# Kernel tuning notes

Measured on AMD Instinct MI355X. Metric: run time of the kernel, lower is better.

The kernel has to match this reference:

```python
import jax, jax.numpy as jnp
import numpy as np

N_NODES = 100000
N_EDGES = 1600000
IN_F = 128
OUT_F = 64
BN_EPS = 1e-5


def setup_inputs() -> dict:
    key = jax.random.key(0)
    ks = jax.random.split(key, 6)
    feature = jax.random.normal(ks[0], (N_NODES, IN_F), dtype=jnp.float32)
    src = jax.random.randint(ks[1], (N_EDGES,), 0, N_NODES, dtype=jnp.int32)
    dst = jax.random.randint(ks[2], (N_EDGES,), 0, N_NODES, dtype=jnp.int32)
    W = jax.random.normal(ks[3], (IN_F, OUT_F), dtype=jnp.float32) * 0.05
    b = jnp.zeros((OUT_F,), dtype=jnp.float32)
    res_W = jax.random.normal(ks[4], (IN_F, OUT_F), dtype=jnp.float32) * 0.05
    res_b = jnp.zeros((OUT_F,), dtype=jnp.float32)
    gamma = jnp.ones((OUT_F,), dtype=jnp.float32)
    beta = jnp.zeros((OUT_F,), dtype=jnp.float32)
    return {"feature": feature, "src": src, "dst": dst, "W": W, "b": b,
            "res_W": res_W, "res_b": res_b, "gamma": gamma, "beta": beta,
            "idx": 0}


def _gcn_layer(feature, src, dst, W, b, res_W, res_b, gamma, beta):
    n = feature.shape[0]
    ones = jnp.ones_like(src, dtype=feature.dtype)
    # DGL norm='both': src-side uses out-degree, dst-side uses in-degree,
    # degrees clamped to min 1 (allow_zero_in_degree=True).
    out_deg = jax.ops.segment_sum(ones, src, num_segments=n)
    in_deg = jax.ops.segment_sum(ones, dst, num_segments=n)
    norm_src = jax.lax.rsqrt(jnp.maximum(out_deg, 1.0))  # [N]
    norm_dst = jax.lax.rsqrt(jnp.maximum(in_deg, 1.0))   # [N]

    # in_feats (128) > out_feats (64): DGL multiplies by W before aggregation.
    h = (feature * norm_src[:, None]) @ W                 # [N, OUT_F]
    agg = jax.ops.segment_sum(h[src], dst, num_segments=n)  # [N, OUT_F]
    conv = jax.nn.relu(agg * norm_dst[:, None] + b)

    # residual connection: activation(Linear(feature))
    res = jax.nn.relu(feature @ res_W + res_b)
    y = conv + res

    # BatchNorm1d (training mode, biased variance)
    mean = jnp.mean(y, axis=0)
    var = jnp.mean(jnp.square(y - mean), axis=0)
    y = (y - mean) * jax.lax.rsqrt(var + BN_EPS) * gamma + beta
    return y


def reference(feature, src, dst, W, b, res_W, res_b, gamma, beta, idx):
    # idx == 0 -> dropout branch is skipped (eval-deterministic reference)
    return _gcn_layer(feature, src, dst, W, b, res_W, res_b, gamma, beta)
```

## Files before the change

### kernel.cpp

```cpp
#include <hip/hip_runtime.h>
#include <hip/hip_fp16.h>

#define NCOL 64
#define KDIM 128
#define NB 512
#define CH 2048

typedef short bf16x8 __attribute__((ext_vector_type(8)));
typedef float f32x4 __attribute__((ext_vector_type(4)));
typedef float f32x2 __attribute__((ext_vector_type(2)));

__device__ __forceinline__ unsigned short f2bf(float f) {
    unsigned int u = __float_as_uint(f);
    return (unsigned short)((u + 0x7fffu + ((u >> 16) & 1u)) >> 16);
}

__global__ __launch_bounds__(256) void coarse_hist(const int* __restrict__ src,
                                                   const int* __restrict__ dst,
                                                   int* __restrict__ outcnt,
                                                   int* __restrict__ bcnt, int E) {
    __shared__ int lh[NB];
    int tid = threadIdx.x;
    for (int i = tid; i < NB; i += 256) lh[i] = 0;
    __syncthreads();
    int i = blockIdx.x * blockDim.x + tid;
    int stride = gridDim.x * blockDim.x;
    for (int e = i; e < E; e += stride) {
        atomicAdd(&outcnt[src[e]], 1);
        atomicAdd(&lh[dst[e] >> 8], 1);
    }
    __syncthreads();
    for (int k = tid; k < NB; k += 256) {
        int c = lh[k];
        if (c) atomicAdd(&bcnt[k], c);
    }
}

__global__ __launch_bounds__(256) void bucket_scan(const int* __restrict__ bcnt,
                                                   int* __restrict__ bbase, int* __restrict__ bcur,
                                                   int* __restrict__ row_start, int N, int E) {
    __shared__ int wsum[8];
    int tid = threadIdx.x, lane = tid & 63, wv = tid >> 6;
    int a = bcnt[tid], b = bcnt[tid + 256];
    int ia = a, ib = b;
#pragma unroll
    for (int off = 1; off < 64; off <<= 1) {
        int t = __shfl_up(ia, off); if (lane >= off) ia += t;
        int u = __shfl_up(ib, off); if (lane >= off) ib += u;
    }
    if (lane == 63) { wsum[wv] = ia; wsum[4 + wv] = ib; }
    __syncthreads();
    if (tid == 0) { int run = 0; for (int i = 0; i < 8; ++i) { int t = wsum[i]; wsum[i] = run; run += t; } }
    __syncthreads();
    int ea = wsum[wv] + ia - a;
    int eb = wsum[4 + wv] + ib - b;
    bbase[tid] = ea; bcur[tid] = ea;
    bbase[tid + 256] = eb; bcur[tid + 256] = eb;
    if (tid == 0) row_start[N] = E;
}

__global__ __launch_bounds__(256) void partition_kernel(
    const int* __restrict__ src, const int* __restrict__ dst,
    int* __restrict__ bcur, uint2* __restrict__ pairs, int E) {
    __shared__ int hist[NB];
    __shared__ int lbase[NB];
    __shared__ int gbase[NB];
    __shared__ int lcur[NB];
    __shared__ uint2 sp[CH];
    __shared__ int wsum[8];

    int tid = threadIdx.x, lane = tid & 63, wv = tid >> 6;
    int c0 = blockIdx.x * CH;
    int cnt = min(CH, E - c0);

    for (int i = tid; i < NB; i += 256) hist[i] = 0;
    __syncthreads();
    for (int i = tid; i < cnt; i += 256)
        atomicAdd(&hist[dst[c0 + i] >> 8], 1);
    __syncthreads();

    {
        int a = hist[tid], b = hist[tid + 256];
        int ia = a, ib = b;
#pragma unroll
        for (int off = 1; off < 64; off <<= 1) {
            int t = __shfl_up(ia, off); if (lane >= off) ia += t;
            int u = __shfl_up(ib, off); if (lane >= off) ib += u;
        }
        if (lane == 63) { wsum[wv] = ia; wsum[4 + wv] = ib; }
        __syncthreads();
        if (tid == 0) { int run = 0; for (int i = 0; i < 8; ++i) { int t = wsum[i]; wsum[i] = run; run += t; } }
        __syncthreads();
        lbase[tid] = wsum[wv] + ia - a;
        lbase[tid + 256] = wsum[4 + wv] + ib - b;
    }
    __syncthreads();

    for (int k = tid; k < NB; k += 256) {
        int c = hist[k];
        gbase[k] = c ? atomicAdd(&bcur[k], c) : 0;
        lcur[k] = lbase[k];
    }
    __syncthreads();

    for (int i = tid; i < cnt; i += 256) {
        int s = src[c0 + i], d = dst[c0 + i];
        int p = atomicAdd(&lcur[d >> 8], 1);
        sp[p] = make_uint2((unsigned)s, (unsigned)d);
    }
    __syncthreads();

    for (int i = tid; i < cnt; i += 256) {
        uint2 p = sp[i];
        int k = (int)(p.y >> 8);
        pairs[gbase[k] + (i - lbase[k])] = p;
    }
}

__global__ __launch_bounds__(256) void fine_kernel(
    const uint2* __restrict__ pairs, const int* __restrict__ bbase,
    int* __restrict__ row_start, int* __restrict__ ssrc, int E, int nbuck, int N) {
    __shared__ int hist[256];
    __shared__ int cur[256];
    __shared__ int wsum[4];
    int k = blockIdx.x;
    int tid = threadIdx.x, lane = tid & 63, wv = tid >> 6;
    int b0 = bbase[k];
    int b1 = (k + 1 < nbuck) ? bbase[k + 1] : E;

    hist[tid] = 0;
    __syncthreads();
    for (int i = b0 + tid; i < b1; i += 256)
        atomicAdd(&hist[pairs[i].y & 255], 1);
    __syncthreads();

    int x = hist[tid], inc = x;
#pragma unroll
    for (int off = 1; off < 64; off <<= 1) {
        int t = __shfl_up(inc, off); if (lane >= off) inc += t;
    }
    if (lane == 63) wsum[wv] = inc;
    __syncthreads();
    if (tid == 0) { int run = 0; for (int i = 0; i < 4; ++i) { int t = wsum[i]; wsum[i] = run; run += t; } }
    __syncthreads();
    int excl = wsum[wv] + inc - x;

    int d = (k << 8) + tid;
    if (d < N) row_start[d] = b0 + excl;
    cur[tid] = b0 + excl;
    __syncthreads();

    for (int i = b0 + tid; i < b1; i += 256) {
        uint2 p = pairs[i];
        int pos = atomicAdd(&cur[p.y & 255], 1);
        ssrc[pos] = (int)p.x;
    }
}

__global__ __launch_bounds__(256) void matmul_mfma(
    const float* __restrict__ feat, const float* __restrict__ W,
    const float* __restrict__ RW, const float* __restrict__ res_b,
    const int* __restrict__ outcnt,
    unsigned int* __restrict__ hb8, float* __restrict__ y, int N) {
    __shared__ bf16x8 Bf[2048];
    int tid = threadIdx.x;
    for (int idx = tid; idx < 2048; idx += 256) {
        int mat = idx >> 10;
        int kc = (idx >> 8) & 3;
        int ct = (idx >> 6) & 3;
        int l = idx & 63;
        const float* Wp = mat ? RW : W;
        int kbase = kc * 32 + (l >> 4) * 8;
        int col = ct * 16 + (l & 15);
        bf16x8 t;
#pragma unroll
        for (int j = 0; j < 8; ++j)
            t[j] = (short)f2bf(Wp[(size_t)(kbase + j) * NCOL + col]);
        Bf[idx] = t;
    }
    __syncthreads();

    int lane = tid & 63;
    int wid = tid >> 6;
    int wave = blockIdx.x * 4 + wid;
    int nwaves = gridDim.x * 4;
    int ntiles = (N + 15) >> 4;
    int c16 = lane & 15, kg = lane >> 4;

    float rbv[4];
#pragma unroll
    for (int ct = 0; ct < 4; ++ct) rbv[ct] = res_b[ct * 16 + c16];

    for (int tile = wave; tile < ntiles; tile += nwaves) {
        int tb = tile << 4;
        f32x4 acch[4], accr[4];
#pragma unroll
        for (int ct = 0; ct < 4; ++ct) {
            acch[ct] = (f32x4){0.f, 0.f, 0.f, 0.f};
            accr[ct] = (f32x4){0.f, 0.f, 0.f, 0.f};
        }

        int arow = tb + c16; if (arow >= N) arow = N - 1;
        const float* fp = feat + (size_t)arow * KDIM + kg * 8;
#pragma unroll
        for (int kc = 0; kc < 4; ++kc) {
            float4 a0 = *(const float4*)(fp + kc * 32);
            float4 a1 = *(const float4*)(fp + kc * 32 + 4);
            bf16x8 af;
            af[0] = (short)f2bf(a0.x); af[1] = (short)f2bf(a0.y);
            af[2] = (short)f2bf(a0.z); af[3] = (short)f2bf(a0.w);
            af[4] = (short)f2bf(a1.x); af[5] = (short)f2bf(a1.y);
            af[6] = (short)f2bf(a1.z); af[7] = (short)f2bf(a1.w);
#pragma unroll
            for (int ct = 0; ct < 4; ++ct) {
                acch[ct] = __builtin_amdgcn_mfma_f32_16x16x32_bf16(
                    af, Bf[(kc * 4 + ct) * 64 + lane], acch[ct], 0, 0, 0);
                accr[ct] = __builtin_amdgcn_mfma_f32_16x16x32_bf16(
                    af, Bf[1024 + (kc * 4 + ct) * 64 + lane], accr[ct], 0, 0, 0);
            }
        }

        float nrm[4];
#pragma unroll
        for (int r = 0; r < 4; ++r) {
            int rw = tb + kg * 4 + r; if (rw >= N) rw = N - 1;
            nrm[r] = rsqrtf(fmaxf((float)outcnt[rw], 1.0f));
        }
#pragma unroll
        for (int r = 0; r < 4; ++r) {
            int row = tb + kg * 4 + r;
            if (row < N) {
                unsigned int p = 0;
                p = (unsigned int)__builtin_amdgcn_cvt_pk_fp8_f32(
                        acch[0][r] * nrm[r], acch[1][r] * nrm[r], (int)p, false);
                p = (unsigned int)__builtin_amdgcn_cvt_pk_fp8_f32(
                        acch[2][r] * nrm[r], acch[3][r] * nrm[r], (int)p, true);
#pragma unroll
                for (int ct = 0; ct < 4; ++ct)
                    y[(size_t)row * NCOL + ct * 16 + c16] = fmaxf(accr[ct][r] + rbv[ct], 0.0f);
                hb8[(size_t)row * 16 + c16] = p;
            }
        }
    }
}

#define GATHER_ROW_STEP(eBase, eEnd, A0, A1, A2, A3)                                   \
    {                                                                                   \
        int e0 = (eBase) + e4, e1 = e0 + 4;                                             \
        int i0 = (e0 < (eEnd)) ? ssrc[e0] : -1;                                         \
        int i1 = (e1 < (eEnd)) ? ssrc[e1] : -1;                                         \
        unsigned int v0 = (i0 >= 0) ? hb8[(size_t)i0 * 16 + dw] : 0u;                   \
        unsigned int v1 = (i1 >= 0) ? hb8[(size_t)i1 * 16 + dw] : 0u;                   \
        f32x2 l0 = __builtin_amdgcn_cvt_pk_f32_fp8((int)v0, false);                     \
        f32x2 h0 = __builtin_amdgcn_cvt_pk_f32_fp8((int)v0, true);                      \
        f32x2 l1 = __builtin_amdgcn_cvt_pk_f32_fp8((int)v1, false);                     \
        f32x2 h1 = __builtin_amdgcn_cvt_pk_f32_fp8((int)v1, true);                      \
        A0 += l0[0] + l1[0]; A1 += l0[1] + l1[1];                                       \
        A2 += h0[0] + h1[0]; A3 += h0[1] + h1[1];                                       \
    }

__global__ __launch_bounds__(256) void gather_kernel(
    const int* __restrict__ row_start, const int* __restrict__ ssrc,
    const unsigned int* __restrict__ hb8, const float* __restrict__ b,
    float* __restrict__ y, float* __restrict__ stats, int N) {
    int tid = threadIdx.x, lane = tid & 63, wid = tid >> 6;
    int e4 = lane >> 4, dw = lane & 15;
    int rowSel = e4 >> 1;
    int colLo = ((e4 & 1) << 5) + dw;
    int wave = blockIdx.x * 4 + wid;
    int nwaves = gridDim.x * 4;

    float bcLo = b[colLo], bcHi = b[colLo + 16];
    float bnLo = 0.f, bnHi = 0.f, bnsqLo = 0.f, bnsqHi = 0.f;

    for (int d0 = wave * 2; d0 < N; d0 += 2 * nwaves) {
        int d1 = d0 + 1;
        int a0 = row_start[d0], a1 = row_start[d0 + 1];
        int b0e = 0, b1e = 0;
        if (d1 < N) { b0e = a1; b1e = row_start[d1 + 1]; }

        float A0 = 0.f, A1 = 0.f, A2 = 0.f, A3 = 0.f;
        float B0 = 0.f, B1 = 0.f, B2 = 0.f, B3 = 0.f;
        int nit = max((a1 - a0 + 7) >> 3, (b1e - b0e + 7) >> 3);
        for (int it = 0; it < nit; ++it) {
            GATHER_ROW_STEP(a0 + it * 8, a1, A0, A1, A2, A3)
            GATHER_ROW_STEP(b0e + it * 8, b1e, B0, B1, B2, B3)
        }

#pragma unroll
        for (int off = 16; off <= 32; off <<= 1) {
            A0 += __shfl_xor(A0, off); A1 += __shfl_xor(A1, off);
            A2 += __shfl_xor(A2, off); A3 += __shfl_xor(A3, off);
            B0 += __shfl_xor(B0, off); B1 += __shfl_xor(B1, off);
            B2 += __shfl_xor(B2, off); B3 += __shfl_xor(B3, off);
        }

        int dd = d0 + rowSel;
        if (dd < N) {
            int deg = rowSel ? (b1e - b0e) : (a1 - a0);
            float nd = rsqrtf(fmaxf((float)deg, 1.0f));
            float vLo = rowSel ? ((e4 & 1) ? B2 : B0) : ((e4 & 1) ? A2 : A0);
            float vHi = rowSel ? ((e4 & 1) ? B3 : B1) : ((e4 & 1) ? A3 : A1);
            float* yp = &y[(size_t)dd * NCOL + colLo];
            float v0 = fmaxf(vLo * nd + bcLo, 0.f) + yp[0];
            float v1 = fmaxf(vHi * nd + bcHi, 0.f) + yp[16];
            yp[0] = v0;
            yp[16] = v1;
            bnLo += v0; bnsqLo += v0 * v0;
            bnHi += v1; bnsqHi += v1 * v1;
        }
    }

    bnLo += __shfl_xor(bnLo, 32); bnsqLo += __shfl_xor(bnsqLo, 32);
    bnHi += __shfl_xor(bnHi, 32); bnsqHi += __shfl_xor(bnsqHi, 32);

    __shared__ float bnred[4][128];
    if (lane < 32) {
        bnred[wid][colLo] = bnLo;
        bnred[wid][colLo + 16] = bnHi;
        bnred[wid][64 + colLo] = bnsqLo;
        bnred[wid][64 + colLo + 16] = bnsqHi;
    }
    __syncthreads();
    if (tid < 128) {
        float v = bnred[0][tid] + bnred[1][tid] + bnred[2][tid] + bnred[3][tid];
        unsafeAtomicAdd(&stats[tid], v);
    }
}

__global__ void bnparam_kernel(const float* __restrict__ gamma, const float* __restrict__ beta,
                               float* __restrict__ stats, float invN) {
    int c = threadIdx.x;
    float mean = stats[c] * invN;
    float var = stats[64 + c] * invN - mean * mean;
    float s = gamma[c] * rsqrtf(var + 1e-5f);
    stats[128 + c] = s;
    stats[192 + c] = beta[c] - mean * s;
}

__global__ __launch_bounds__(256) void apply_kernel(float* __restrict__ y,
                                                    const float* __restrict__ stats, int total4) {
    int i = blockIdx.x * blockDim.x + threadIdx.x;
    int stride = gridDim.x * blockDim.x;
    float4* y4 = (float4*)y;
    for (; i < total4; i += stride) {
        float4 v = y4[i];
        int cbase = (i & 15) << 2;
        float4 s = *(const float4*)&stats[128 + cbase];
        float4 t = *(const float4*)&stats[192 + cbase];
        v.x = v.x * s.x + t.x;
        v.y = v.y * s.y + t.y;
        v.z = v.z * s.z + t.z;
        v.w = v.w * s.w + t.w;
        y4[i] = v;
    }
}

extern "C" void kernel_launch(void* const* d_in, const int* in_sizes, int n_in,
                              void* d_out, int out_size, void* d_ws, size_t ws_size,
                              hipStream_t stream) {
    const float* feat  = (const float*)d_in[0];
    const int*   src   = (const int*)d_in[1];
    const int*   dst   = (const int*)d_in[2];
    const float* W     = (const float*)d_in[3];
    const float* b     = (const float*)d_in[4];
    const float* RW    = (const float*)d_in[5];
    const float* rb    = (const float*)d_in[6];
    const float* gamma = (const float*)d_in[7];
    const float* beta  = (const float*)d_in[8];

    int N = in_sizes[0] / KDIM;
    int E = in_sizes[1];
    float* out = (float*)d_out;
    int nbuck = (N + 255) >> 8;

    char* wsb = (char*)d_ws;
    unsigned int* hb8 = (unsigned int*)wsb;                wsb += (size_t)N * 16 * 4;
    uint2* pairs    = (uint2*)wsb;                         wsb += (size_t)E * 8;
    int*   ssrc     = (int*)wsb;                           wsb += (size_t)E * 4;
    int*   row_start= (int*)wsb;                           wsb += (size_t)(N + 1) * 4;
    int*   outcnt   = (int*)wsb;                           wsb += (size_t)N * 4;
    float* stats    = (float*)wsb;                         wsb += 256 * 4;
    int*   bcnt     = (int*)wsb;                           wsb += NB * 4;
    int*   bbase    = (int*)wsb;                           wsb += NB * 4;
    int*   bcur     = (int*)wsb;

    hipMemsetAsync(outcnt, 0, ((size_t)N + 256 + NB) * 4, stream);

    coarse_hist<<<1024, 256, 0, stream>>>(src, dst, outcnt, bcnt, E);
    bucket_scan<<<1, 256, 0, stream>>>(bcnt, bbase, bcur, row_start, N, E);
    matmul_mfma<<<512, 256, 0, stream>>>(feat, W, RW, rb, outcnt, hb8, out, N);
    partition_kernel<<<(E + CH - 1) / CH, 256, 0, stream>>>(src, dst, bcur, pairs, E);
    fine_kernel<<<nbuck, 256, 0, stream>>>(pairs, bbase, row_start, ssrc, E, nbuck, N);
    gather_kernel<<<2048, 256, 0, stream>>>(row_start, ssrc, hb8, b, out, stats, N);
    bnparam_kernel<<<1, 64, 0, stream>>>(gamma, beta, stats, 1.0f / (float)N);
    apply_kernel<<<2048, 256, 0, stream>>>(out, stats, (N * NCOL) / 4);
}
```

Measured before the change: 278.1 us.

## Pack edge pairs into 32-bit words, fold degree count into partition, fuse BN param

Moves the source out-degree atomics from coarse_hist into partition_kernel, so coarse_hist only reads dst. Packs each (src, dst-low-byte) pair into one 32-bit word, halving partition/fine scratch traffic; the 17-bit src field holds indices below 131072, enough for N = 100000. The matmul now launches one wave per tile instead of a grid-stride loop, the gather unrolls four edges per step instead of two for more memory-level parallelism, and the BN parameter kernel is folded into apply_kernel, which removes one launch. Risks are higher register pressure in gather and a recomputation of the BN parameters in every apply block.

```diff
diff --git a/kernel.cpp b/kernel.cpp
--- a/kernel.cpp
+++ b/kernel.cpp
@@ -15,9 +15,7 @@
     return (unsigned short)((u + 0x7fffu + ((u >> 16) & 1u)) >> 16);
 }
 
-__global__ __launch_bounds__(256) void coarse_hist(const int* __restrict__ src,
-                                                   const int* __restrict__ dst,
-                                                   int* __restrict__ outcnt,
+__global__ __launch_bounds__(256) void coarse_hist(const int* __restrict__ dst,
                                                    int* __restrict__ bcnt, int E) {
     __shared__ int lh[NB];
     int tid = threadIdx.x;
@@ -25,10 +23,8 @@
     __syncthreads();
     int i = blockIdx.x * blockDim.x + tid;
     int stride = gridDim.x * blockDim.x;
-    for (int e = i; e < E; e += stride) {
-        atomicAdd(&outcnt[src[e]], 1);
+    for (int e = i; e < E; e += stride)
         atomicAdd(&lh[dst[e] >> 8], 1);
-    }
     __syncthreads();
     for (int k = tid; k < NB; k += 256) {
         int c = lh[k];
@@ -61,7 +57,8 @@
 
 __global__ __launch_bounds__(256) void partition_kernel(
     const int* __restrict__ src, const int* __restrict__ dst,
-    int* __restrict__ bcur, uint2* __restrict__ pairs, int E) {
+    int* __restrict__ bcur, unsigned int* __restrict__ pk,
+    int* __restrict__ outcnt, int E) {
     __shared__ int hist[NB];
     __shared__ int lbase[NB];
     __shared__ int gbase[NB];
@@ -105,6 +102,7 @@
 
     for (int i = tid; i < cnt; i += 256) {
         int s = src[c0 + i], d = dst[c0 + i];
+        atomicAdd(&outcnt[s], 1);
         int p = atomicAdd(&lcur[d >> 8], 1);
         sp[p] = make_uint2((unsigned)s, (unsigned)d);
     }
@@ -113,12 +111,12 @@
     for (int i = tid; i < cnt; i += 256) {
         uint2 p = sp[i];
         int k = (int)(p.y >> 8);
-        pairs[gbase[k] + (i - lbase[k])] = p;
+        pk[gbase[k] + (i - lbase[k])] = ((p.y & 255u) << 17) | p.x;
     }
 }
 
 __global__ __launch_bounds__(256) void fine_kernel(
-    const uint2* __restrict__ pairs, const int* __restrict__ bbase,
+    const unsigned int* __restrict__ pk, const int* __restrict__ bbase,
     int* __restrict__ row_start, int* __restrict__ ssrc, int E, int nbuck, int N) {
     __shared__ int hist[256];
     __shared__ int cur[256];
@@ -131,7 +129,7 @@
     hist[tid] = 0;
     __syncthreads();
     for (int i = b0 + tid; i < b1; i += 256)
-        atomicAdd(&hist[pairs[i].y & 255], 1);
+        atomicAdd(&hist[pk[i] >> 17], 1);
     __syncthreads();
 
     int x = hist[tid], inc = x;
@@ -151,9 +149,9 @@
     __syncthreads();
 
     for (int i = b0 + tid; i < b1; i += 256) {
-        uint2 p = pairs[i];
-        int pos = atomicAdd(&cur[p.y & 255], 1);
-        ssrc[pos] = (int)p.x;
+        unsigned int p = pk[i];
+        int pos = atomicAdd(&cur[p >> 17], 1);
+        ssrc[pos] = (int)(p & 0x1FFFFu);
     }
 }
 
@@ -182,81 +180,89 @@
 
     int lane = tid & 63;
     int wid = tid >> 6;
-    int wave = blockIdx.x * 4 + wid;
-    int nwaves = gridDim.x * 4;
     int ntiles = (N + 15) >> 4;
+    int tile = blockIdx.x * 4 + wid;
+    if (tile >= ntiles) return;
     int c16 = lane & 15, kg = lane >> 4;
 
     float rbv[4];
 #pragma unroll
     for (int ct = 0; ct < 4; ++ct) rbv[ct] = res_b[ct * 16 + c16];
 
-    for (int tile = wave; tile < ntiles; tile += nwaves) {
-        int tb = tile << 4;
-        f32x4 acch[4], accr[4];
+    int tb = tile << 4;
+    f32x4 acch[4], accr[4];
+#pragma unroll
+    for (int ct = 0; ct < 4; ++ct) {
+        acch[ct] = (f32x4){0.f, 0.f, 0.f, 0.f};
+        accr[ct] = (f32x4){0.f, 0.f, 0.f, 0.f};
+    }
+
+    int arow = tb + c16; if (arow >= N) arow = N - 1;
+    const float* fp = feat + (size_t)arow * KDIM + kg * 8;
+#pragma unroll
+    for (int kc = 0; kc < 4; ++kc) {
+        float4 a0 = *(const float4*)(fp + kc * 32);
+        float4 a1 = *(const float4*)(fp + kc * 32 + 4);
+        bf16x8 af;
+        af[0] = (short)f2bf(a0.x); af[1] = (short)f2bf(a0.y);
+        af[2] = (short)f2bf(a0.z); af[3] = (short)f2bf(a0.w);
+        af[4] = (short)f2bf(a1.x); af[5] = (short)f2bf(a1.y);
+        af[6] = (short)f2bf(a1.z); af[7] = (short)f2bf(a1.w);
 #pragma unroll
         for (int ct = 0; ct < 4; ++ct) {
-            acch[ct] = (f32x4){0.f, 0.f, 0.f, 0.f};
-            accr[ct] = (f32x4){0.f, 0.f, 0.f, 0.f};
-        }
-
-        int arow = tb + c16; if (arow >= N) arow = N - 1;
-        const float* fp = feat + (size_t)arow * KDIM + kg * 8;
-#pragma unroll
-        for (int kc = 0; kc < 4; ++kc) {
-            float4 a0 = *(const float4*)(fp + kc * 32);
-            float4 a1 = *(const float4*)(fp + kc * 32 + 4);
-            bf16x8 af;
-            af[0] = (short)f2bf(a0.x); af[1] = (short)f2bf(a0.y);
-            af[2] = (short)f2bf(a0.z); af[3] = (short)f2bf(a0.w);
-            af[4] = (short)f2bf(a1.x); af[5] = (short)f2bf(a1.y);
-            af[6] = (short)f2bf(a1.z); af[7] = (short)f2bf(a1.w);
-#pragma unroll
-            for (int ct = 0; ct < 4; ++ct) {
-                acch[ct] = __builtin_amdgcn_mfma_f32_16x16x32_bf16(
-                    af, Bf[(kc * 4 + ct) * 64 + lane], acch[ct], 0, 0, 0);
-                accr[ct] = __builtin_amdgcn_mfma_f32_16x16x32_bf16(
-                    af, Bf[1024 + (kc * 4 + ct) * 64 + lane], accr[ct], 0, 0, 0);
-            }
-        }
-
-        float nrm[4];
-#pragma unroll
-        for (int r = 0; r < 4; ++r) {
-            int rw = tb + kg * 4 + r; if (rw >= N) rw = N - 1;
-            nrm[r] = rsqrtf(fmaxf((float)outcnt[rw], 1.0f));
-        }
-#pragma unroll
-        for (int r = 0; r < 4; ++r) {
-            int row = tb + kg * 4 + r;
-            if (row < N) {
-                unsigned int p = 0;
-                p = (unsigned int)__builtin_amdgcn_cvt_pk_fp8_f32(
-                        acch[0][r] * nrm[r], acch[1][r] * nrm[r], (int)p, false);
-                p = (unsigned int)__builtin_amdgcn_cvt_pk_fp8_f32(
-                        acch[2][r] * nrm[r], acch[3][r] * nrm[r], (int)p, true);
-#pragma unroll
-                for (int ct = 0; ct < 4; ++ct)
-                    y[(size_t)row * NCOL + ct * 16 + c16] = fmaxf(accr[ct][r] + rbv[ct], 0.0f);
-                hb8[(size_t)row * 16 + c16] = p;
-            }
+            acch[ct] = __builtin_amdgcn_mfma_f32_16x16x32_bf16(
+                af, Bf[(kc * 4 + ct) * 64 + lane], acch[ct], 0, 0, 0);
+            accr[ct] = __builtin_amdgcn_mfma_f32_16x16x32_bf16(
+                af, Bf[1024 + (kc * 4 + ct) * 64 + lane], accr[ct], 0, 0, 0);
+        }
+    }
+
+    float nrm[4];
+#pragma unroll
+    for (int r = 0; r < 4; ++r) {
+        int rw = tb + kg * 4 + r; if (rw >= N) rw = N - 1;
+        nrm[r] = rsqrtf(fmaxf((float)outcnt[rw], 1.0f));
+    }
+#pragma unroll
+    for (int r = 0; r < 4; ++r) {
+        int row = tb + kg * 4 + r;
+        if (row < N) {
+            unsigned int p = 0;
+            p = (unsigned int)__builtin_amdgcn_cvt_pk_fp8_f32(
+                    acch[0][r] * nrm[r], acch[1][r] * nrm[r], (int)p, false);
+            p = (unsigned int)__builtin_amdgcn_cvt_pk_fp8_f32(
+                    acch[2][r] * nrm[r], acch[3][r] * nrm[r], (int)p, true);
+#pragma unroll
+            for (int ct = 0; ct < 4; ++ct)
+                y[(size_t)row * NCOL + ct * 16 + c16] = fmaxf(accr[ct][r] + rbv[ct], 0.0f);
+            hb8[(size_t)row * 16 + c16] = p;
         }
     }
 }
 
 #define GATHER_ROW_STEP(eBase, eEnd, A0, A1, A2, A3)                                   \
     {                                                                                   \
-        int e0 = (eBase) + e4, e1 = e0 + 4;                                             \
+        int e0 = (eBase) + e4, e1 = e0 + 4, e2 = e0 + 8, e3 = e0 + 12;                  \
         int i0 = (e0 < (eEnd)) ? ssrc[e0] : -1;                                         \
         int i1 = (e1 < (eEnd)) ? ssrc[e1] : -1;                                         \
+        int i2 = (e2 < (eEnd)) ? ssrc[e2] : -1;                                         \
+        int i3 = (e3 < (eEnd)) ? ssrc[e3] : -1;                                         \
         unsigned int v0 = (i0 >= 0) ? hb8[(size_t)i0 * 16 + dw] : 0u;                   \
         unsigned int v1 = (i1 >= 0) ? hb8[(size_t)i1 * 16 + dw] : 0u;                   \
+        unsigned int v2 = (i2 >= 0) ? hb8[(size_t)i2 * 16 + dw] : 0u;                   \
+        unsigned int v3 = (i3 >= 0) ? hb8[(size_t)i3 * 16 + dw] : 0u;                   \
         f32x2 l0 = __builtin_amdgcn_cvt_pk_f32_fp8((int)v0, false);                     \
         f32x2 h0 = __builtin_amdgcn_cvt_pk_f32_fp8((int)v0, true);                      \
         f32x2 l1 = __builtin_amdgcn_cvt_pk_f32_fp8((int)v1, false);                     \
         f32x2 h1 = __builtin_amdgcn_cvt_pk_f32_fp8((int)v1, true);                      \
-        A0 += l0[0] + l1[0]; A1 += l0[1] + l1[1];                                       \
-        A2 += h0[0] + h1[0]; A3 += h0[1] + h1[1];                                       \
+        f32x2 l2 = __builtin_amdgcn_cvt_pk_f32_fp8((int)v2, false);                     \
+        f32x2 h2 = __builtin_amdgcn_cvt_pk_f32_fp8((int)v2, true);                      \
+        f32x2 l3 = __builtin_amdgcn_cvt_pk_f32_fp8((int)v3, false);                     \
+        f32x2 h3 = __builtin_amdgcn_cvt_pk_f32_fp8((int)v3, true);                      \
+        A0 += (l0[0] + l1[0]) + (l2[0] + l3[0]);                                        \
+        A1 += (l0[1] + l1[1]) + (l2[1] + l3[1]);                                        \
+        A2 += (h0[0] + h1[0]) + (h2[0] + h3[0]);                                        \
+        A3 += (h0[1] + h1[1]) + (h2[1] + h3[1]);                                        \
     }
 
 __global__ __launch_bounds__(256) void gather_kernel(
@@ -281,10 +287,10 @@
 
         float A0 = 0.f, A1 = 0.f, A2 = 0.f, A3 = 0.f;
         float B0 = 0.f, B1 = 0.f, B2 = 0.f, B3 = 0.f;
-        int nit = max((a1 - a0 + 7) >> 3, (b1e - b0e + 7) >> 3);
+        int nit = max((a1 - a0 + 15) >> 4, (b1e - b0e + 15) >> 4);
         for (int it = 0; it < nit; ++it) {
-            GATHER_ROW_STEP(a0 + it * 8, a1, A0, A1, A2, A3)
-            GATHER_ROW_STEP(b0e + it * 8, b1e, B0, B1, B2, B3)
+            GATHER_ROW_STEP(a0 + it * 16, a1, A0, A1, A2, A3)
+            GATHER_ROW_STEP(b0e + it * 16, b1e, B0, B1, B2, B3)
         }
 
 #pragma unroll
@@ -328,26 +334,29 @@
     }
 }
 
-__global__ void bnparam_kernel(const float* __restrict__ gamma, const float* __restrict__ beta,
-                               float* __restrict__ stats, float invN) {
-    int c = threadIdx.x;
-    float mean = stats[c] * invN;
-    float var = stats[64 + c] * invN - mean * mean;
-    float s = gamma[c] * rsqrtf(var + 1e-5f);
-    stats[128 + c] = s;
-    stats[192 + c] = beta[c] - mean * s;
-}
-
 __global__ __launch_bounds__(256) void apply_kernel(float* __restrict__ y,
-                                                    const float* __restrict__ stats, int total4) {
-    int i = blockIdx.x * blockDim.x + threadIdx.x;
+                                                    const float* __restrict__ stats,
+                                                    const float* __restrict__ gamma,
+                                                    const float* __restrict__ beta,
+                                                    float invN, int total4) {
+    __shared__ float sc[64], sh[64];
+    int tid = threadIdx.x;
+    if (tid < 64) {
+        float mean = stats[tid] * invN;
+        float var = stats[64 + tid] * invN - mean * mean;
+        float s = gamma[tid] * rsqrtf(var + 1e-5f);
+        sc[tid] = s;
+        sh[tid] = beta[tid] - mean * s;
+    }
+    __syncthreads();
+    int i = blockIdx.x * blockDim.x + tid;
     int stride = gridDim.x * blockDim.x;
     float4* y4 = (float4*)y;
     for (; i < total4; i += stride) {
         float4 v = y4[i];
         int cbase = (i & 15) << 2;
-        float4 s = *(const float4*)&stats[128 + cbase];
-        float4 t = *(const float4*)&stats[192 + cbase];
+        float4 s = *(const float4*)&sc[cbase];
+        float4 t = *(const float4*)&sh[cbase];
         v.x = v.x * s.x + t.x;
         v.y = v.y * s.y + t.y;
         v.z = v.z * s.z + t.z;
@@ -376,7 +385,7 @@
 
     char* wsb = (char*)d_ws;
     unsigned int* hb8 = (unsigned int*)wsb;                wsb += (size_t)N * 16 * 4;
-    uint2* pairs    = (uint2*)wsb;                         wsb += (size_t)E * 8;
+    unsigned int* pk  = (unsigned int*)wsb;                wsb += (size_t)E * 4;
     int*   ssrc     = (int*)wsb;                           wsb += (size_t)E * 4;
     int*   row_start= (int*)wsb;                           wsb += (size_t)(N + 1) * 4;
     int*   outcnt   = (int*)wsb;                           wsb += (size_t)N * 4;
@@ -387,12 +396,11 @@
 
     hipMemsetAsync(outcnt, 0, ((size_t)N + 256 + NB) * 4, stream);
 
-    coarse_hist<<<1024, 256, 0, stream>>>(src, dst, outcnt, bcnt, E);
+    coarse_hist<<<512, 256, 0, stream>>>(dst, bcnt, E);
     bucket_scan<<<1, 256, 0, stream>>>(bcnt, bbase, bcur, row_start, N, E);
-    matmul_mfma<<<512, 256, 0, stream>>>(feat, W, RW, rb, outcnt, hb8, out, N);
-    partition_kernel<<<(E + CH - 1) / CH, 256, 0, stream>>>(src, dst, bcur, pairs, E);
-    fine_kernel<<<nbuck, 256, 0, stream>>>(pairs, bbase, row_start, ssrc, E, nbuck, N);
+    partition_kernel<<<(E + CH - 1) / CH, 256, 0, stream>>>(src, dst, bcur, pk, outcnt, E);
+    matmul_mfma<<<(((N + 15) >> 4) + 3) / 4, 256, 0, stream>>>(feat, W, RW, rb, outcnt, hb8, out, N);
+    fine_kernel<<<nbuck, 256, 0, stream>>>(pk, bbase, row_start, ssrc, E, nbuck, N);
     gather_kernel<<<2048, 256, 0, stream>>>(row_start, ssrc, hb8, b, out, stats, N);
-    bnparam_kernel<<<1, 64, 0, stream>>>(gamma, beta, stats, 1.0f / (float)N);
-    apply_kernel<<<2048, 256, 0, stream>>>(out, stats, (N * NCOL) / 4);
-}
+    apply_kernel<<<2048, 256, 0, stream>>>(out, stats, gamma, beta, 1.0f / (float)N, (N * NCOL) / 4);
+}
```

After: 263.8 us. -5.1%, faster.
